# Optimization experiments

Measured on AMD Instinct MI355X. Metric: run time of the kernel, lower is better.

Reference implementation:

```python
import jax, jax.numpy as jnp
import numpy as np

B, L, DIM = 2, 2048, 1024
H, DH, W = 16, 64, 256  # heads, head_dim, window_size
ROPE_BASE = 10000.0


def _rope(x):
    # x: [b, l, h, d] -> rotate consecutive pairs (torch view_as_complex semantics)
    l, d = x.shape[1], x.shape[3]
    freqs = 1.0 / (ROPE_BASE ** (jnp.arange(0, d, 2, dtype=jnp.float32) / d))  # [d/2]
    ang = jnp.arange(l, dtype=jnp.float32)[:, None] * freqs[None, :]           # [l, d/2]
    cos = jnp.cos(ang)[None, :, None, :].astype(x.dtype)
    sin = jnp.sin(ang)[None, :, None, :].astype(x.dtype)
    xe, xo = x[..., 0::2], x[..., 1::2]
    ye = xe * cos - xo * sin
    yo = xe * sin + xo * cos
    return jnp.stack([ye, yo], axis=-1).reshape(x.shape)


def setup_inputs() -> dict:
    key = jax.random.key(0)
    ks = jax.random.split(key, 7)
    sh = (B, L, DIM)
    return {
        "q": jax.random.normal(ks[0], sh, jnp.float32),
        "k": jax.random.normal(ks[1], sh, jnp.float32),
        "v": jax.random.normal(ks[2], sh, jnp.float32),
        "wq": jax.random.normal(ks[3], (H * DH, DIM), jnp.float32) * 0.02,
        "wk": jax.random.normal(ks[4], (H * DH, DIM), jnp.float32) * 0.02,
        "wv": jax.random.normal(ks[5], (H * DH, DIM), jnp.float32) * 0.02,
        "wo": jax.random.normal(ks[6], (DIM, H * DH), jnp.float32) * 0.02,
    }


def reference(q, k, v, wq, wk, wv, wo):
    b, l, _ = q.shape
    qh = (q @ wq.T).reshape(b, l, H, DH)
    kh = (k @ wk.T).reshape(b, l, H, DH)
    vh = (v @ wv.T).reshape(b, l, H, DH).transpose(0, 2, 1, 3)  # [b,h,l,d]
    qh = _rope(qh).transpose(0, 2, 1, 3)                        # [b,h,l,d]
    kh = _rope(kh).transpose(0, 2, 1, 3)
    scores = jnp.einsum('bhqd,bhkd->bhqk', qh, kh) * (DH ** -0.5)
    i = jnp.arange(l)[:, None]
    j = jnp.arange(l)[None, :]
    window_mask = (j <= i) & (j >= i - W)  # keys in [i-W, i], matches the loop
    scores = jnp.where(window_mask, scores, -1e30)
    probs = jax.nn.softmax(scores, axis=-1)
    out = jnp.einsum('bhqk,bhkd->bhqd', probs, vh)
    out = out.transpose(0, 2, 1, 3).reshape(b, l, H * DH)
    return out @ wo.T
```

## Files before the change

### kernel.cpp

```cpp
#include <hip/hip_runtime.h>
#include <stdint.h>

#define B_    2
#define L_    2048
#define DIM_  1024
#define H_    16
#define DH_   64
#define WWIN  256

typedef __attribute__((ext_vector_type(4))) float f32x4;
typedef __attribute__((ext_vector_type(8))) short bf16x8;

__device__ __forceinline__ unsigned short f2bf(float x) {
  union { float f; unsigned u; } c; c.f = x;
  unsigned r = c.u + 0x7fffu + ((c.u >> 16) & 1u);
  return (unsigned short)(r >> 16);
}

struct CastArgs {
  const float* src[7];
  unsigned short* dst[7];
};
__global__ __launch_bounds__(256) void cast_bf16_kernel(CastArgs a) {
  int bid = blockIdx.x;
  int arr, base;
  if (bid < 12288) {
    arr = bid >> 12;
    base = (bid & 4095) << 10;
  } else {
    int t = bid - 12288;
    arr = 3 + (t >> 10);
    base = (t & 1023) << 10;
  }
  int i = base + (int)threadIdx.x * 4;
  float4 v = *(const float4*)(a.src[arr] + i);
  ushort4 o;
  o.x = f2bf(v.x); o.y = f2bf(v.y); o.z = f2bf(v.z); o.w = f2bf(v.w);
  *(ushort4*)(a.dst[arr] + i) = o;
}

#define BM 128
#define BN 64
#define BK 64

__device__ __forceinline__ void gld_lds16(const void* g, void* l) {
  __builtin_amdgcn_global_load_lds(
      (const __attribute__((address_space(1))) void*)g,
      (__attribute__((address_space(3))) void*)l, 16, 0, 0);
}

__device__ __forceinline__ void gemm_core_128x128(
    const unsigned short* __restrict__ A, const unsigned short* __restrict__ Bt,
    unsigned short* As, unsigned short* Bs, f32x4 (&acc)[4][4],
    int m0, int n0) {
  const int tid = threadIdx.x;
  const int wave = tid >> 6, lane = tid & 63;
  const int quad = lane >> 4, l16 = lane & 15;
  const int wm = wave >> 1, wn = wave & 1;
  const int srow = tid >> 3, sc = tid & 7;

  for (int k = 0; k < 16; ++k) {
    const int k0 = k * 64;
    #pragma unroll
    for (int rd = 0; rd < 4; ++rd) {
      int row = rd * 32 + srow;
      int cs = sc ^ (row & 7);
      gld_lds16(A + (size_t)(m0 + row) * 1024 + k0 + cs * 8, As + row * 64 + sc * 8);
    }
    #pragma unroll
    for (int rd = 0; rd < 4; ++rd) {
      int row = rd * 32 + srow;
      int cs = sc ^ (row & 7);
      gld_lds16(Bt + (size_t)(n0 + row) * 1024 + k0 + cs * 8, Bs + row * 64 + sc * 8);
    }
    __syncthreads();
    #pragma unroll
    for (int ks = 0; ks < 2; ++ks) {
      bf16x8 af[4], bfr[4];
      #pragma unroll
      for (int i = 0; i < 4; ++i) {
        int row = wm * 64 + i * 16 + l16;
        int ch = (ks * 4 + quad) ^ (row & 7);
        af[i] = *(const bf16x8*)(As + row * 64 + ch * 8);
      }
      #pragma unroll
      for (int j = 0; j < 4; ++j) {
        int row = wn * 64 + j * 16 + l16;
        int ch = (ks * 4 + quad) ^ (row & 7);
        bfr[j] = *(const bf16x8*)(Bs + row * 64 + ch * 8);
      }
      #pragma unroll
      for (int i = 0; i < 4; ++i)
        #pragma unroll
        for (int j = 0; j < 4; ++j)
          acc[i][j] = __builtin_amdgcn_mfma_f32_16x16x32_bf16(af[i], bfr[j], acc[i][j], 0, 0, 0);
    }
    __syncthreads();
  }
}

__device__ __forceinline__ void gemm_core_1024(
    const unsigned short* __restrict__ A, const unsigned short* __restrict__ Bt,
    unsigned short* As, unsigned short* Bs, f32x4 (&acc)[2][4],
    int m0, int n0) {
  const int tid = threadIdx.x;
  const int wave = tid >> 6, lane = tid & 63;
  const int quad = lane >> 4, l16 = lane & 15;
  const int srow = tid >> 3, sc = tid & 7;

  auto stage = [&](int k0, int buf) {
    unsigned short* Ad = As + buf * 8192;
    unsigned short* Bd = Bs + buf * 4096;
    #pragma unroll
    for (int rd = 0; rd < 4; ++rd) {
      int row = rd * 32 + srow;
      int cs = sc ^ (row & 7);
      gld_lds16(A + (size_t)(m0 + row) * 1024 + k0 + cs * 8, Ad + row * BK + sc * 8);
    }
    #pragma unroll
    for (int rd = 0; rd < 2; ++rd) {
      int row = rd * 32 + srow;
      int cs = sc ^ (row & 7);
      gld_lds16(Bt + (size_t)(n0 + row) * 1024 + k0 + cs * 8, Bd + row * BK + sc * 8);
    }
  };

  stage(0, 0);
  for (int k = 0; k < 16; ++k) {
    const int cur = k & 1;
    __syncthreads();
    if (k < 15) stage((k + 1) * BK, cur ^ 1);
    const unsigned short* Ac = As + cur * 8192;
    const unsigned short* Bc = Bs + cur * 4096;
    #pragma unroll
    for (int ks = 0; ks < 2; ++ks) {
      bf16x8 af[2], bfr[4];
      #pragma unroll
      for (int i = 0; i < 2; ++i) {
        int row = wave * 32 + i * 16 + l16;
        int ch = (ks * 4 + quad) ^ (row & 7);
        af[i] = *(const bf16x8*)(Ac + row * BK + ch * 8);
      }
      #pragma unroll
      for (int j = 0; j < 4; ++j) {
        int row = j * 16 + l16;
        int ch = (ks * 4 + quad) ^ (row & 7);
        bfr[j] = *(const bf16x8*)(Bc + row * BK + ch * 8);
      }
      #pragma unroll
      for (int i = 0; i < 2; ++i)
        #pragma unroll
        for (int j = 0; j < 4; ++j)
          acc[i][j] = __builtin_amdgcn_mfma_f32_16x16x32_bf16(af[i], bfr[j], acc[i][j], 0, 0, 0);
    }
  }
}

struct ProjArgs {
  const unsigned short* A[3];
  const unsigned short* Bt[3];
  unsigned short* C[3];
};
__global__ __launch_bounds__(256) void gemm_proj_kernel(ProjArgs pa) {
  __shared__ unsigned short SH[16384];
  unsigned short* As = SH;
  unsigned short* Bs = SH + 8192;

  const int bflat = blockIdx.x;
  const int xcd = bflat & 7, s = bflat >> 3;
  const int nblk = s & 7;
  const int mz = xcd * 12 + (s >> 3);
  const int z = mz >> 5;
  const int mblk = mz & 31;
  const int m0 = mblk * BM, n0 = nblk * 128;

  f32x4 acc[4][4] = {};
  gemm_core_128x128(pa.A[z], pa.Bt[z], As, Bs, acc, m0, n0);

  const int tid = threadIdx.x;
  const int lane = tid & 63, wave = tid >> 6;
  const int quad = lane >> 4, l16 = lane & 15;
  const int wm = wave >> 1, wn = wave & 1;
  const int h = nblk * 2 + wn;

  if (z < 2) {
    float frev[4];
    #pragma unroll
    for (int j = 0; j < 4; ++j) {
      int d = j * 16 + l16;
      frev[j] = exp2f(-(float)(d >> 1) * 0.41524101186092029f) * 0.15915494309189535f;
    }
    unsigned short* C = pa.C[z];
    const bool even = (l16 & 1) == 0;
    #pragma unroll
    for (int i = 0; i < 4; ++i)
      #pragma unroll
      for (int r = 0; r < 4; ++r) {
        int m = m0 + wm * 64 + i * 16 + quad * 4 + r;
        int b = m >> 11, l = m & (L_ - 1);
        float lf = (float)l;
        #pragma unroll
        for (int j = 0; j < 4; ++j) {
          int d = j * 16 + l16;
          float v = acc[i][j][r];
          float p = __shfl_xor(v, 1);
          float a = lf * frev[j];
          float t = a - floorf(a);
          float sn = __builtin_amdgcn_sinf(t);
          float cs = __builtin_amdgcn_cosf(t);
          float o = even ? (v * cs - p * sn) : (p * sn + v * cs);
          C[(((size_t)b * H_ + h) * L_ + l) * DH_ + d] = f2bf(o);
        }
      }
  } else {
    char* T = (char*)SH + wave * 8192;
    #pragma unroll
    for (int i = 0; i < 4; ++i)
      #pragma unroll
      for (int j = 0; j < 4; ++j) {
        int d = j * 16 + l16;
        int mb = i * 32 + quad * 8;
        int ch = mb >> 4, sub = mb & 15;
        uint2 pk;
        pk.x = (unsigned)f2bf(acc[i][j][0]) | ((unsigned)f2bf(acc[i][j][1]) << 16);
        pk.y = (unsigned)f2bf(acc[i][j][2]) | ((unsigned)f2bf(acc[i][j][3]) << 16);
        *(uint2*)(T + d * 128 + ((ch ^ (d & 7)) << 4) + sub) = pk;
      }
    asm volatile("s_waitcnt lgkmcnt(0)" ::: "memory");
    int b = m0 >> 11;
    int lbase = (m0 & (L_ - 1)) + wm * 64;
    unsigned short* C = pa.C[2];
    #pragma unroll
    for (int t = 0; t < 8; ++t) {
      int d = t * 8 + (lane >> 3);
      int ch = lane & 7;
      uint4 o = *(uint4*)(T + d * 128 + ((ch ^ (d & 7)) << 4));
      *(uint4*)(C + (((size_t)b * H_ + h) * DH_ + d) * L_ + lbase + ch * 8) = o;
    }
  }
}

__global__ __launch_bounds__(256) void gemm_out_kernel(
    const unsigned short* __restrict__ A, const unsigned short* __restrict__ Bt,
    float* __restrict__ C) {
  __shared__ unsigned short SH[24576];
  unsigned short* As = SH;
  unsigned short* Bs = SH + 16384;

  const int bflat = blockIdx.x;
  const int xcd = bflat & 7, s = bflat >> 3;
  const int nblk = s & 15;
  const int mblk = xcd * 4 + (s >> 4);
  const int m0 = mblk * BM, n0 = nblk * BN;

  f32x4 acc[2][4] = {};
  gemm_core_1024(A, Bt, As, Bs, acc, m0, n0);

  const int lane = threadIdx.x & 63, wave = threadIdx.x >> 6;
  const int quad = lane >> 4, l16 = lane & 15;
  #pragma unroll
  for (int i = 0; i < 2; ++i)
    #pragma unroll
    for (int j = 0; j < 4; ++j)
      #pragma unroll
      for (int r = 0; r < 4; ++r) {
        int m = m0 + wave * 32 + i * 16 + quad * 4 + r;
        int n = n0 + j * 16 + l16;
        C[(size_t)m * DIM_ + n] = acc[i][j][r];
      }
}

#define NCH 20
__global__ __launch_bounds__(256) void attn_kernel(
    const unsigned short* __restrict__ Qh,
    const unsigned short* __restrict__ Kh,
    const unsigned short* __restrict__ Vt,
    unsigned short* __restrict__ O) {
  __shared__ unsigned short KVs[64 * 168];
  __shared__ unsigned short Ps[4][16 * 172];
  const int tid = threadIdx.x;
  const int wave = tid >> 6, lane = tid & 63;
  const int quad = lane >> 4, l16 = lane & 15;

  const int bflat = blockIdx.x;
  const int xcd = bflat & 7, s = bflat >> 3;
  const int qt = s >> 2;
  const int bh = xcd * 4 + (s & 3);

  const int q0 = qt * 64;
  const int kwin0 = q0 - WWIN;
  const int qb = q0 + wave * 16;
  const bool edge = (kwin0 < 0);

  bf16x8 qf0, qf1;
  {
    const unsigned short* qrow = Qh + ((size_t)bh * L_ + qb + l16) * DH_;
    qf0 = *(const bf16x8*)(qrow + quad * 8);
    qf1 = *(const bf16x8*)(qrow + 32 + quad * 8);
  }

  f32x4 S[NCH] = {};

  const int srow = tid >> 3, sc = tid & 7;
  #pragma unroll
  for (int half = 0; half < 2; ++half) {
    __syncthreads();
    #pragma unroll
    for (int rep = 0; rep < 5; ++rep) {
      int row = rep * 32 + srow;
      int key = kwin0 + half * 160 + row;
      key = key < 0 ? 0 : key;
      int cs = sc ^ (row & 7);
      gld_lds16(Kh + ((size_t)bh * L_ + key) * DH_ + cs * 8,
                (unsigned short*)KVs + row * 64 + sc * 8);
    }
    __syncthreads();
    #pragma unroll
    for (int cc = 0; cc < 10; ++cc) {
      const int c = half * 10 + cc;
      if (c < wave || c > wave + 16) continue;
      int row = cc * 16 + l16;
      const unsigned short* kr = (const unsigned short*)KVs + row * 64;
      bf16x8 kf0 = *(const bf16x8*)(kr + ((quad) ^ (row & 7)) * 8);
      bf16x8 kf1 = *(const bf16x8*)(kr + ((4 + quad) ^ (row & 7)) * 8);
      S[c] = __builtin_amdgcn_mfma_f32_16x16x32_bf16(qf0, kf0, S[c], 0, 0, 0);
      S[c] = __builtin_amdgcn_mfma_f32_16x16x32_bf16(qf1, kf1, S[c], 0, 0, 0);
    }
  }

  float inv_l[4];
  #pragma unroll
  for (int r = 0; r < 4; ++r) {
    const int i = qb + quad * 4 + r;
    float mx = -1e30f;
    #pragma unroll
    for (int c = 0; c < NCH; ++c) {
      if (c < wave || c > wave + 16) continue;
      float v = S[c][r];
      if (edge || c == wave || c == wave + 16) {
        int key = kwin0 + c * 16 + l16;
        bool valid = (key >= 0) && (key <= i) && (key >= i - WWIN);
        v = valid ? v : -1e30f;
        S[c][r] = v;
      }
      mx = fmaxf(mx, v);
    }
    mx = fmaxf(mx, __shfl_xor(mx, 1));
    mx = fmaxf(mx, __shfl_xor(mx, 2));
    mx = fmaxf(mx, __shfl_xor(mx, 4));
    mx = fmaxf(mx, __shfl_xor(mx, 8));
    float sum = 0.f;
    #pragma unroll
    for (int c = 0; c < NCH; ++c) {
      if (c < wave || c > wave + 16) continue;
      float e = __builtin_amdgcn_exp2f((S[c][r] - mx) * 0.18033688011112042f);
      S[c][r] = e;
      sum += e;
    }
    sum += __shfl_xor(sum, 1);
    sum += __shfl_xor(sum, 2);
    sum += __shfl_xor(sum, 4);
    sum += __shfl_xor(sum, 8);
    inv_l[r] = 1.0f / sum;
  }

  f32x4 Oacc[4] = {};
  unsigned short* pw = &Ps[wave][0];
  #pragma unroll
  for (int half = 0; half < 2; ++half) {
    const int glo = (half == 0) ? (wave >> 1) : 0;
    const int ghi = (half == 0) ? 4 : ((wave + 6) >> 1);
    __syncthreads();
    for (int rep = 0; rep < 5; ++rep) {
      int ci = rep * 256 + tid;
      int row = ci / 20, c = ci % 20;
      int key0 = kwin0 + half * 160 + c * 8;
      uint4 val = {0, 0, 0, 0};
      if (key0 >= 0)
        val = *(const uint4*)(Vt + ((size_t)bh * DH_ + row) * L_ + key0);
      *(uint4*)(&KVs[row * 168 + c * 8]) = val;
    }
    #pragma unroll
    for (int cc = 0; cc < 10; ++cc) {
      if ((cc >> 1) < glo || (cc >> 1) > ghi) continue;
      #pragma unroll
      for (int r = 0; r < 4; ++r) {
        float p = S[half * 10 + cc][r] * inv_l[r];
        pw[(quad * 4 + r) * 172 + cc * 16 + l16] = f2bf(p);
      }
    }
    __syncthreads();
    #pragma unroll
    for (int s5 = 0; s5 < 5; ++s5) {
      if (s5 < glo || s5 > ghi) continue;
      bf16x8 pf = *(const bf16x8*)(pw + l16 * 172 + s5 * 32 + quad * 8);
      int lk = s5 * 32 + quad * 8;
      #pragma unroll
      for (int t = 0; t < 4; ++t) {
        bf16x8 vf = *(const bf16x8*)(&KVs[(t * 16 + l16) * 168 + lk]);
        Oacc[t] = __builtin_amdgcn_mfma_f32_16x16x32_bf16(pf, vf, Oacc[t], 0, 0, 0);
      }
    }
  }

  int b = bh >> 4, h = bh & 15;
  #pragma unroll
  for (int t = 0; t < 4; ++t)
    #pragma unroll
    for (int r = 0; r < 4; ++r) {
      int l = qb + quad * 4 + r;
      int col = h * DH_ + t * 16 + l16;
      O[((size_t)b * L_ + l) * (H_ * DH_) + col] = f2bf(Oacc[t][r]);
    }
}

extern "C" void kernel_launch(void* const* d_in, const int* in_sizes, int n_in,
                              void* d_out, int out_size, void* d_ws, size_t ws_size,
                              hipStream_t stream) {
  const float* q  = (const float*)d_in[0];
  const float* k  = (const float*)d_in[1];
  const float* v  = (const float*)d_in[2];
  const float* wq = (const float*)d_in[3];
  const float* wk = (const float*)d_in[4];
  const float* wv = (const float*)d_in[5];
  const float* wo = (const float*)d_in[6];

  const size_t SA = (size_t)B_ * L_ * DIM_;
  const size_t SW = (size_t)DIM_ * DIM_;
  unsigned short* w   = (unsigned short*)d_ws;
  unsigned short* qb  = w; w += SA;
  unsigned short* kb  = w; w += SA;
  unsigned short* vb  = w; w += SA;
  unsigned short* wqb = w; w += SW;
  unsigned short* wkb = w; w += SW;
  unsigned short* wvb = w; w += SW;
  unsigned short* wob = w; w += SW;
  unsigned short* qh  = w; w += SA;
  unsigned short* kh  = w; w += SA;
  unsigned short* vt  = w; w += SA;
  unsigned short* Ob  = w; w += SA;

  CastArgs ca;
  ca.src[0] = q;  ca.dst[0] = qb;
  ca.src[1] = k;  ca.dst[1] = kb;
  ca.src[2] = v;  ca.dst[2] = vb;
  ca.src[3] = wq; ca.dst[3] = wqb;
  ca.src[4] = wk; ca.dst[4] = wkb;
  ca.src[5] = wv; ca.dst[5] = wvb;
  ca.src[6] = wo; ca.dst[6] = wob;
  cast_bf16_kernel<<<dim3(16384), 256, 0, stream>>>(ca);

  ProjArgs pa;
  pa.A[0] = qb; pa.Bt[0] = wqb; pa.C[0] = qh;
  pa.A[1] = kb; pa.Bt[1] = wkb; pa.C[1] = kh;
  pa.A[2] = vb; pa.Bt[2] = wvb; pa.C[2] = vt;
  gemm_proj_kernel<<<dim3(768), 256, 0, stream>>>(pa);

  attn_kernel<<<dim3(32 * 32), 256, 0, stream>>>(qh, kh, vt, Ob);
  gemm_out_kernel<<<dim3(16 * 32), 256, 0, stream>>>(Ob, wob, (float*)d_out);
}
```

Before: 199.7 us.

## Double-buffer 128x128 GEMM core and use it for output projection

The 128x128 GEMM core used by the QKV projection now double-buffers its LDS tiles, prefetching the next K slice while the current one is computed, and the per-iteration trailing barrier is dropped. The output projection switches from a 128x64 tile with 512 blocks to the shared 128x128 core with 256 blocks, and the separate 128x64 core is removed. This hides global load latency and halves B-tile reloads in the output GEMM. In exchange LDS usage doubles to 64KB per block, which may lower occupancy, and the output GEMM has fewer blocks on a 256-CU part. A barrier is added before the V epilogue reuses shared memory.

```diff
diff --git a/kernel.cpp b/kernel.cpp
--- a/kernel.cpp
+++ b/kernel.cpp
@@ -40,8 +40,6 @@
 }
 
 #define BM 128
-#define BN 64
-#define BK 64
 
 __device__ __forceinline__ void gld_lds16(const void* g, void* l) {
   __builtin_amdgcn_global_load_lds(
@@ -59,21 +57,30 @@
   const int wm = wave >> 1, wn = wave & 1;
   const int srow = tid >> 3, sc = tid & 7;
 
-  for (int k = 0; k < 16; ++k) {
-    const int k0 = k * 64;
+  auto stage = [&](int k0, int buf) {
+    unsigned short* Ad = As + buf * 8192;
+    unsigned short* Bd = Bs + buf * 8192;
     #pragma unroll
     for (int rd = 0; rd < 4; ++rd) {
       int row = rd * 32 + srow;
       int cs = sc ^ (row & 7);
-      gld_lds16(A + (size_t)(m0 + row) * 1024 + k0 + cs * 8, As + row * 64 + sc * 8);
+      gld_lds16(A + (size_t)(m0 + row) * 1024 + k0 + cs * 8, Ad + row * 64 + sc * 8);
     }
     #pragma unroll
     for (int rd = 0; rd < 4; ++rd) {
       int row = rd * 32 + srow;
       int cs = sc ^ (row & 7);
-      gld_lds16(Bt + (size_t)(n0 + row) * 1024 + k0 + cs * 8, Bs + row * 64 + sc * 8);
-    }
-    __syncthreads();
+      gld_lds16(Bt + (size_t)(n0 + row) * 1024 + k0 + cs * 8, Bd + row * 64 + sc * 8);
+    }
+  };
+
+  stage(0, 0);
+  for (int k = 0; k < 16; ++k) {
+    const int cur = k & 1;
+    __syncthreads();
+    if (k < 15) stage((k + 1) * 64, cur ^ 1);
+    const unsigned short* Ac = As + cur * 8192;
+    const unsigned short* Bc = Bs + cur * 8192;
     #pragma unroll
     for (int ks = 0; ks < 2; ++ks) {
       bf16x8 af[4], bfr[4];
@@ -81,74 +88,16 @@
       for (int i = 0; i < 4; ++i) {
         int row = wm * 64 + i * 16 + l16;
         int ch = (ks * 4 + quad) ^ (row & 7);
-        af[i] = *(const bf16x8*)(As + row * 64 + ch * 8);
+        af[i] = *(const bf16x8*)(Ac + row * 64 + ch * 8);
       }
       #pragma unroll
       for (int j = 0; j < 4; ++j) {
         int row = wn * 64 + j * 16 + l16;
         int ch = (ks * 4 + quad) ^ (row & 7);
-        bfr[j] = *(const bf16x8*)(Bs + row * 64 + ch * 8);
+        bfr[j] = *(const bf16x8*)(Bc + row * 64 + ch * 8);
       }
       #pragma unroll
       for (int i = 0; i < 4; ++i)
-        #pragma unroll
-        for (int j = 0; j < 4; ++j)
-          acc[i][j] = __builtin_amdgcn_mfma_f32_16x16x32_bf16(af[i], bfr[j], acc[i][j], 0, 0, 0);
-    }
-    __syncthreads();
-  }
-}
-
-__device__ __forceinline__ void gemm_core_1024(
-    const unsigned short* __restrict__ A, const unsigned short* __restrict__ Bt,
-    unsigned short* As, unsigned short* Bs, f32x4 (&acc)[2][4],
-    int m0, int n0) {
-  const int tid = threadIdx.x;
-  const int wave = tid >> 6, lane = tid & 63;
-  const int quad = lane >> 4, l16 = lane & 15;
-  const int srow = tid >> 3, sc = tid & 7;
-
-  auto stage = [&](int k0, int buf) {
-    unsigned short* Ad = As + buf * 8192;
-    unsigned short* Bd = Bs + buf * 4096;
-    #pragma unroll
-    for (int rd = 0; rd < 4; ++rd) {
-      int row = rd * 32 + srow;
-      int cs = sc ^ (row & 7);
-      gld_lds16(A + (size_t)(m0 + row) * 1024 + k0 + cs * 8, Ad + row * BK + sc * 8);
-    }
-    #pragma unroll
-    for (int rd = 0; rd < 2; ++rd) {
-      int row = rd * 32 + srow;
-      int cs = sc ^ (row & 7);
-      gld_lds16(Bt + (size_t)(n0 + row) * 1024 + k0 + cs * 8, Bd + row * BK + sc * 8);
-    }
-  };
-
-  stage(0, 0);
-  for (int k = 0; k < 16; ++k) {
-    const int cur = k & 1;
-    __syncthreads();
-    if (k < 15) stage((k + 1) * BK, cur ^ 1);
-    const unsigned short* Ac = As + cur * 8192;
-    const unsigned short* Bc = Bs + cur * 4096;
-    #pragma unroll
-    for (int ks = 0; ks < 2; ++ks) {
-      bf16x8 af[2], bfr[4];
-      #pragma unroll
-      for (int i = 0; i < 2; ++i) {
-        int row = wave * 32 + i * 16 + l16;
-        int ch = (ks * 4 + quad) ^ (row & 7);
-        af[i] = *(const bf16x8*)(Ac + row * BK + ch * 8);
-      }
-      #pragma unroll
-      for (int j = 0; j < 4; ++j) {
-        int row = j * 16 + l16;
-        int ch = (ks * 4 + quad) ^ (row & 7);
-        bfr[j] = *(const bf16x8*)(Bc + row * BK + ch * 8);
-      }
-      #pragma unroll
-      for (int i = 0; i < 2; ++i)
         #pragma unroll
         for (int j = 0; j < 4; ++j)
           acc[i][j] = __builtin_amdgcn_mfma_f32_16x16x32_bf16(af[i], bfr[j], acc[i][j], 0, 0, 0);
@@ -162,9 +111,9 @@
   unsigned short* C[3];
 };
 __global__ __launch_bounds__(256) void gemm_proj_kernel(ProjArgs pa) {
-  __shared__ unsigned short SH[16384];
+  __shared__ unsigned short SH[32768];
   unsigned short* As = SH;
-  unsigned short* Bs = SH + 8192;
+  unsigned short* Bs = SH + 16384;
 
   const int bflat = blockIdx.x;
   const int xcd = bflat & 7, s = bflat >> 3;
@@ -213,6 +162,7 @@
         }
       }
   } else {
+    __syncthreads();
     char* T = (char*)SH + wave * 8192;
     #pragma unroll
     for (int i = 0; i < 4; ++i)
@@ -243,29 +193,30 @@
 __global__ __launch_bounds__(256) void gemm_out_kernel(
     const unsigned short* __restrict__ A, const unsigned short* __restrict__ Bt,
     float* __restrict__ C) {
-  __shared__ unsigned short SH[24576];
+  __shared__ unsigned short SH[32768];
   unsigned short* As = SH;
   unsigned short* Bs = SH + 16384;
 
   const int bflat = blockIdx.x;
   const int xcd = bflat & 7, s = bflat >> 3;
-  const int nblk = s & 15;
-  const int mblk = xcd * 4 + (s >> 4);
-  const int m0 = mblk * BM, n0 = nblk * BN;
-
-  f32x4 acc[2][4] = {};
-  gemm_core_1024(A, Bt, As, Bs, acc, m0, n0);
+  const int nblk = s & 7;
+  const int mblk = xcd * 4 + (s >> 3);
+  const int m0 = mblk * BM, n0 = nblk * 128;
+
+  f32x4 acc[4][4] = {};
+  gemm_core_128x128(A, Bt, As, Bs, acc, m0, n0);
 
   const int lane = threadIdx.x & 63, wave = threadIdx.x >> 6;
   const int quad = lane >> 4, l16 = lane & 15;
+  const int wm = wave >> 1, wn = wave & 1;
   #pragma unroll
-  for (int i = 0; i < 2; ++i)
+  for (int i = 0; i < 4; ++i)
     #pragma unroll
     for (int j = 0; j < 4; ++j)
       #pragma unroll
       for (int r = 0; r < 4; ++r) {
-        int m = m0 + wave * 32 + i * 16 + quad * 4 + r;
-        int n = n0 + j * 16 + l16;
+        int m = m0 + wm * 64 + i * 16 + quad * 4 + r;
+        int n = n0 + wn * 64 + j * 16 + l16;
         C[(size_t)m * DIM_ + n] = acc[i][j][r];
       }
 }
@@ -457,5 +408,5 @@
   gemm_proj_kernel<<<dim3(768), 256, 0, stream>>>(pa);
 
   attn_kernel<<<dim3(32 * 32), 256, 0, stream>>>(qh, kh, vt, Ob);
-  gemm_out_kernel<<<dim3(16 * 32), 256, 0, stream>>>(Ob, wob, (float*)d_out);
-}
+  gemm_out_kernel<<<dim3(256), 256, 0, stream>>>(Ob, wob, (float*)d_out);
+}
```

After: 196.4 us. Within noise of the previous version (-1.7%).
